# Performance work log

Hardware: AMD Instinct MI355X
Metric: run time of the kernel (lower is better)

Reference implementation:

```python
import jax, jax.numpy as jnp
import numpy as np


def reference(x, phi, sigma, M_phi_plus, M_phi_minus, M_u, padded_sl):
    """STU forward: spectral FFT convolution + autoregressive input term.

    x:   (B, L, D) input sequence
    phi: (L, K) time-domain spectral filters (top-K Hankel eigenvectors);
         V = rfft(phi, n=padded_sl) matches the module's precomputed V.
    sigma: (K,) Hankel eigenvalues
    M_phi_plus/minus: (K, D, D) per-filter projections
    M_u: (k_u, D, D) AR-on-input matrices
    """
    B, L, D = x.shape
    K = sigma.shape[0]
    n = padded_sl  # FFT length for causal linear convolution

    # Alternating-sign trick for the 'minus' featurization:
    # sum_j (-1)^j phi_j u_{t-j} = (-1)^t * conv(phi, sgn*u)_t
    sgn = jnp.where(jnp.arange(L) % 2 == 0, 1.0, -1.0).astype(x.dtype)[None, :, None]  # (1,L,1)

    V = jnp.fft.rfft(phi, n=n, axis=0)                       # (n//2+1, K) complex
    U = jnp.fft.rfft(jnp.stack([x, x * sgn], axis=-1), n=n, axis=1)  # (B, n//2+1, D, 2)
    prod = V[None, :, :, None, None] * U[:, :, None, :, :]    # (B, n//2+1, K, D, 2)
    conv = jnp.fft.irfft(prod, n=n, axis=1)[:, :L]            # (B, L, K, D, 2) causal conv
    U_plus = conv[..., 0]
    U_minus = conv[..., 1] * sgn[..., None]                   # undo sign on output side

    # Fold sigma^{1/4} scaling into the projection matrices.
    sig4 = (sigma ** 0.25).astype(x.dtype)[:, None, None]     # (K,1,1)
    spectral = (
        jnp.einsum('blkd,kdo->blo', U_plus, M_phi_plus * sig4)
        + jnp.einsum('blkd,kdo->blo', U_minus, M_phi_minus * sig4)
    )

    # compute_ar_u: y_t += sum_{i=0}^{k_u-1} x_{t-i} @ M_u[i]  (use_ar_u=True)
    ar_u = jnp.einsum('bld,do->blo', x, M_u[0])
    for i in range(1, M_u.shape[0]):  # small fixed depth k_u=3
        x_shift = jnp.pad(x, ((0, 0), (i, 0), (0, 0)))[:, :L]
        ar_u = ar_u + jnp.einsum('bld,do->blo', x_shift, M_u[i])

    # use_ar_y=False branch; dropout=0 (identity)
    return spectral + ar_u


def setup_inputs() -> dict:
    key = jax.random.key(0)
    ks = jax.random.split(key, 6)
    B, L, D, K, KU, N = 1, 2048, 768, 16, 3, 4096
    x = jax.random.normal(ks[0], (B, L, D), jnp.float32)
    phi = jax.random.normal(ks[1], (L, K), jnp.float32) / np.sqrt(L).astype(np.float32)
    sigma = jax.random.uniform(ks[2], (K,), jnp.float32, 0.1, 1.0)
    M_phi_plus = jax.random.normal(ks[3], (K, D, D), jnp.float32) * 0.02
    M_phi_minus = jax.random.normal(ks[4], (K, D, D), jnp.float32) * 0.02
    M_u = jax.random.normal(ks[5], (KU, D, D), jnp.float32) * 0.02
    return {"x": x, "phi": phi, "sigma": sigma, "M_phi_plus": M_phi_plus,
            "M_phi_minus": M_phi_minus, "M_u": M_u, "padded_sl": N}
```

## Files before the change

kernel.cpp:

```cpp
#include <hip/hip_runtime.h>

typedef __attribute__((ext_vector_type(8))) short bf16x8;
typedef __attribute__((ext_vector_type(4))) float f32x4;

#define SL 2048
#define DM 768
#define MSPEC 24576
#define MTOT  26880

__device__ __forceinline__ short f2bf(float f) {
  unsigned u = __builtin_bit_cast(unsigned, f);
  u = (u + 0x7FFFu + ((u >> 16) & 1u)) >> 16;
  return (short)u;
}

__device__ __forceinline__ void gload16(const short* g, short* l) {
  __builtin_amdgcn_global_load_lds(
      (const __attribute__((address_space(1))) void*)g,
      (__attribute__((address_space(3))) void*)l, 16, 0, 0);
}

__global__ __launch_bounds__(256) void k_front(const float* __restrict__ x,
                                               const float* __restrict__ phi,
                                               float* __restrict__ out,
                                               short* __restrict__ xT,
                                               short* __restrict__ Tmat,
                                               short* __restrict__ U) {
  __shared__ short tile[64 * 65];
  const int wid = blockIdx.x;
  const int t = threadIdx.x;

  if (wid < 1536) {
    reinterpret_cast<float4*>(out)[(size_t)wid * 256 + t] = float4{0.f, 0.f, 0.f, 0.f};

  } else if (wid < 1920) {
    const int b = wid - 1536;
    const int d0 = (b % 12) * 64, l0 = (b / 12) * 64;
#pragma unroll
    for (int rr = 0; rr < 16; ++rr) {
      int ll = rr * 4 + (t >> 6), dl = t & 63;
      tile[ll * 65 + dl] = f2bf(x[(size_t)(l0 + ll) * DM + d0 + dl]);
    }
    __syncthreads();
#pragma unroll
    for (int rr = 0; rr < 16; ++rr) {
      int dl = rr * 4 + (t >> 6), ll = t & 63;
      xT[(size_t)(d0 + dl) * SL + l0 + ll] = tile[ll * 65 + dl];
    }

  } else if (wid < 6016) {
    int g = (wid - 1920) * 256 + t;
    int b8 = g & 15, a = (g >> 4) & 127, dlag = (g >> 11) & 15, c = g >> 15;
    int k = c & 15;
    int jb = dlag * 128 + a - b8 * 8;
    short v[8];
#pragma unroll
    for (int i2 = 0; i2 < 8; ++i2) {
      int j = jb - i2;
      float p = 0.f;
      if (j >= 0) {
        p = phi[j * 16 + k];
        if (c >= 16 && (j & 1)) p = -p;
      }
      v[i2] = f2bf(p);
    }
    *reinterpret_cast<int4*>(Tmat + (size_t)g * 8) = *reinterpret_cast<const int4*>(v);

  } else {
    int g = (wid - 6016) * 256 + t;
    int d8 = g % 96;
    int rest = g / 96;
    int l = rest & 2047, i = rest >> 11;
    int d = d8 * 8;
    short v[8] = {0, 0, 0, 0, 0, 0, 0, 0};
    if (l >= i) {
      const float4* src = reinterpret_cast<const float4*>(x + (size_t)(l - i) * DM + d);
      float4 f0 = src[0], f1 = src[1];
      v[0] = f2bf(f0.x); v[1] = f2bf(f0.y); v[2] = f2bf(f0.z); v[3] = f2bf(f0.w);
      v[4] = f2bf(f1.x); v[5] = f2bf(f1.y); v[6] = f2bf(f1.z); v[7] = f2bf(f1.w);
    }
    *reinterpret_cast<int4*>(U + (size_t)l * MTOT + MSPEC + i * DM + d) =
        *reinterpret_cast<const int4*>(v);
  }
}

__global__ __launch_bounds__(256) void k_mid(const short* __restrict__ Tmat,
                                             const short* __restrict__ xT,
                                             short* __restrict__ U,
                                             const float* __restrict__ Mp,
                                             const float* __restrict__ Mm,
                                             const float* __restrict__ Mu,
                                             const float* __restrict__ sigma,
                                             short* __restrict__ McatT) {
  __shared__ __align__(16) short As[2][128 * 32];
  __shared__ __align__(16) short Bs[2][128 * 32];
  const int wid = blockIdx.x;
  const int t = threadIdx.x;

  if (wid < 3072) {
    const int slot = wid >> 3;
    const int c = (wid & 7) * 4 + (slot & 3);
    const int dtile = (slot >> 2) % 6;
    const int ib = 15 - (slot >> 2) / 6;
    const int lane = t & 63, wave = t >> 6;
    const int wm = (wave >> 1) * 64, wn = (wave & 1) * 64;
    const int lrow = lane & 15, quad = lane >> 4;
    const int l4 = lane >> 2, lq = lane & 3;
    const int r0 = wave * 32 + l4;
    const int swz = (lq ^ ((l4 >> 1) & 3)) * 8;
    const int foff = ((quad ^ ((lrow >> 1) & 3)) << 3);

    f32x4 acc[4][4] = {};
    const short* Abase = Tmat + (((size_t)c * 16) << 14) + r0 * 128 + swz;
    const short* Bbase = xT + (size_t)dtile * 128 * SL + (size_t)r0 * SL + swz;
    const int nit = 4 * (ib + 1);

    auto stage = [&](int it, int buf) {
      int dlag = it >> 2, kk = it & 3;
      const short* Ad = Abase + ((size_t)dlag << 14) + kk * 32;
      const short* Bd = Bbase + (ib - dlag) * 128 + kk * 32;
      short* lA = &As[buf][wave * 1024 + lane * 8];
      short* lB = &Bs[buf][wave * 1024 + lane * 8];
      gload16(Ad, lA);
      gload16(Ad + 16 * 128, lA + 512);
      gload16(Bd, lB);
      gload16(Bd + 16 * SL, lB + 512);
    };

    stage(0, 0);
    int cur = 0;
    for (int it = 0; it < nit; ++it) {
      __syncthreads();
      if (it + 1 < nit) stage(it + 1, cur ^ 1);
      bf16x8 af[4], bfr[4];
#pragma unroll
      for (int im = 0; im < 4; ++im)
        af[im] = *reinterpret_cast<const bf16x8*>(&As[cur][(wm + im * 16 + lrow) * 32 + foff]);
#pragma unroll
      for (int in = 0; in < 4; ++in)
        bfr[in] = *reinterpret_cast<const bf16x8*>(&Bs[cur][(wn + in * 16 + lrow) * 32 + foff]);
#pragma unroll
      for (int im = 0; im < 4; ++im)
#pragma unroll
        for (int in = 0; in < 4; ++in)
          acc[im][in] = __builtin_amdgcn_mfma_f32_16x16x32_bf16(af[im], bfr[in], acc[im][in], 0, 0, 0);
      cur ^= 1;
    }
    const int l0 = ib * 128, colbase = c * DM + dtile * 128;
#pragma unroll
    for (int im = 0; im < 4; ++im)
#pragma unroll
      for (int in = 0; in < 4; ++in)
#pragma unroll
        for (int r4 = 0; r4 < 4; ++r4) {
          int row = wm + im * 16 + quad * 4 + r4;
          int col = wn + in * 16 + lrow;
          U[(size_t)(l0 + row) * MTOT + colbase + col] = f2bf(acc[im][in][r4]);
        }

  } else {
    short* tile = &As[0][0];
    const int idx = wid - 3072;
    const int m0 = (idx % 420) * 64, o0 = (idx / 420) * 64;
#pragma unroll
    for (int rr = 0; rr < 16; ++rr) {
      int ml = rr * 4 + (t >> 6), ol = t & 63;
      int m = m0 + ml, o = o0 + ol;
      float v;
      if (m < MSPEC) {
        int c = m / DM, d = m - c * DM;
        int k = c & 15;
        float s4 = sqrtf(sqrtf(sigma[k]));
        if (c < 16) v = Mp[((size_t)c * DM + d) * DM + o] * s4;
        else        v = Mm[((size_t)(c - 16) * DM + d) * DM + o] * s4;
      } else {
        int mm = m - MSPEC;
        int i = mm / DM, d = mm - i * DM;
        v = Mu[((size_t)i * DM + d) * DM + o];
      }
      tile[ml * 65 + ol] = f2bf(v);
    }
    __syncthreads();
#pragma unroll
    for (int rr = 0; rr < 16; ++rr) {
      int ol = rr * 4 + (t >> 6), ml = t & 63;
      McatT[(size_t)(o0 + ol) * MTOT + m0 + ml] = tile[ml * 65 + ol];
    }
  }
}

__global__ __launch_bounds__(256) void k_gemm2(const short* __restrict__ U,
                                               const short* __restrict__ McatT,
                                               float* __restrict__ out) {
  __shared__ __align__(16) short As[2][128 * 32];
  __shared__ __align__(16) short Bs[2][128 * 32];
  const int wid = blockIdx.x;
  const int kc = wid & 7;
  const int slot = wid >> 3;
  const int otile = slot % 6;
  const int lb = slot / 6;
  const int t = threadIdx.x;
  const int lane = t & 63, wave = t >> 6;
  const int wm = (wave >> 1) * 64, wn = (wave & 1) * 64;
  const int lrow = lane & 15, quad = lane >> 4;
  const int l4 = lane >> 2, lq = lane & 3;
  const int r0 = wave * 32 + l4;
  const int swz = (lq ^ ((l4 >> 1) & 3)) * 8;
  const int foff = ((quad ^ ((lrow >> 1) & 3)) << 3);

  f32x4 acc[4][4] = {};
  const short* Ab = U + (size_t)lb * 128 * MTOT + kc * 3360 + (size_t)r0 * MTOT + swz;
  const short* Bb = McatT + (size_t)otile * 128 * MTOT + kc * 3360 + (size_t)r0 * MTOT + swz;

  auto stage = [&](int s, int buf) {
    short* lA = &As[buf][wave * 1024 + lane * 8];
    short* lB = &Bs[buf][wave * 1024 + lane * 8];
    gload16(Ab + s * 32, lA);
    gload16(Ab + s * 32 + (size_t)16 * MTOT, lA + 512);
    gload16(Bb + s * 32, lB);
    gload16(Bb + s * 32 + (size_t)16 * MTOT, lB + 512);
  };

  stage(0, 0);
  int cur = 0;
  for (int s = 0; s < 105; ++s) {
    __syncthreads();
    if (s + 1 < 105) stage(s + 1, cur ^ 1);
    bf16x8 af[4], bfr[4];
#pragma unroll
    for (int im = 0; im < 4; ++im)
      af[im] = *reinterpret_cast<const bf16x8*>(&As[cur][(wm + im * 16 + lrow) * 32 + foff]);
#pragma unroll
    for (int in = 0; in < 4; ++in)
      bfr[in] = *reinterpret_cast<const bf16x8*>(&Bs[cur][(wn + in * 16 + lrow) * 32 + foff]);
#pragma unroll
    for (int im = 0; im < 4; ++im)
#pragma unroll
      for (int in = 0; in < 4; ++in)
        acc[im][in] = __builtin_amdgcn_mfma_f32_16x16x32_bf16(af[im], bfr[in], acc[im][in], 0, 0, 0);
    cur ^= 1;
  }
  const int l0 = lb * 128, o0 = otile * 128;
#pragma unroll
  for (int im = 0; im < 4; ++im)
#pragma unroll
    for (int in = 0; in < 4; ++in)
#pragma unroll
      for (int r4 = 0; r4 < 4; ++r4) {
        int row = wm + im * 16 + quad * 4 + r4;
        int col = wn + in * 16 + lrow;
        atomicAdd(&out[(size_t)(l0 + row) * DM + o0 + col], acc[im][in][r4]);
      }
}

extern "C" void kernel_launch(void* const* d_in, const int* in_sizes, int n_in,
                              void* d_out, int out_size, void* d_ws, size_t ws_size,
                              hipStream_t stream) {
  (void)in_sizes; (void)n_in; (void)out_size; (void)ws_size;
  const float* x     = (const float*)d_in[0];
  const float* phi   = (const float*)d_in[1];
  const float* sigma = (const float*)d_in[2];
  const float* Mp    = (const float*)d_in[3];
  const float* Mm    = (const float*)d_in[4];
  const float* Mu    = (const float*)d_in[5];
  float* out = (float*)d_out;
  char* ws = (char*)d_ws;

  short* U     = (short*)(ws);
  short* Tmat  = (short*)(ws + 110100480);
  short* xT    = (short*)(ws + 126877696);
  short* McatT = (short*)(ws + 130023424);

  k_front<<<dim3(8320), dim3(256), 0, stream>>>(x, phi, out, xT, Tmat, U);
  k_mid<<<dim3(8112), dim3(256), 0, stream>>>(Tmat, xT, U, Mp, Mm, Mu, sigma, McatT);
  k_gemm2<<<dim3(768), dim3(256), 0, stream>>>(U, McatT, out);
}
```

Before: 444.2 us.

## Fuse spectral GEMM and output GEMM with per-row-block counters for overlap

The McatT transpose/scale work moves into the front kernel, and the Toeplitz GEMM and the projection GEMM are merged into one launch. Output GEMM blocks spin on a per-L-block completion counter that the first-stage blocks increment, so output GEMM work for finished row blocks can overlap the remaining first-stage work. This removes one launch and the tail bubble between the stages. It relies on forward-progress assumptions about block scheduling, since the higher-index waiting blocks must not starve the producers, and it adds spin-wait overhead.

```diff
diff --git a/kernel.cpp b/kernel.cpp
--- a/kernel.cpp
+++ b/kernel.cpp
@@ -7,6 +7,7 @@
 #define DM 768
 #define MSPEC 24576
 #define MTOT  26880
+#define CNT_OFF 171311104
 
 __device__ __forceinline__ short f2bf(float f) {
   unsigned u = __builtin_bit_cast(unsigned, f);
@@ -22,146 +23,22 @@
 
 __global__ __launch_bounds__(256) void k_front(const float* __restrict__ x,
                                                const float* __restrict__ phi,
+                                               const float* __restrict__ Mp,
+                                               const float* __restrict__ Mm,
+                                               const float* __restrict__ Mu,
+                                               const float* __restrict__ sigma,
                                                float* __restrict__ out,
                                                short* __restrict__ xT,
                                                short* __restrict__ Tmat,
-                                               short* __restrict__ U) {
+                                               short* __restrict__ U,
+                                               short* __restrict__ McatT,
+                                               unsigned* __restrict__ cnt) {
   __shared__ short tile[64 * 65];
   const int wid = blockIdx.x;
   const int t = threadIdx.x;
 
-  if (wid < 1536) {
-    reinterpret_cast<float4*>(out)[(size_t)wid * 256 + t] = float4{0.f, 0.f, 0.f, 0.f};
-
-  } else if (wid < 1920) {
-    const int b = wid - 1536;
-    const int d0 = (b % 12) * 64, l0 = (b / 12) * 64;
-#pragma unroll
-    for (int rr = 0; rr < 16; ++rr) {
-      int ll = rr * 4 + (t >> 6), dl = t & 63;
-      tile[ll * 65 + dl] = f2bf(x[(size_t)(l0 + ll) * DM + d0 + dl]);
-    }
-    __syncthreads();
-#pragma unroll
-    for (int rr = 0; rr < 16; ++rr) {
-      int dl = rr * 4 + (t >> 6), ll = t & 63;
-      xT[(size_t)(d0 + dl) * SL + l0 + ll] = tile[ll * 65 + dl];
-    }
-
-  } else if (wid < 6016) {
-    int g = (wid - 1920) * 256 + t;
-    int b8 = g & 15, a = (g >> 4) & 127, dlag = (g >> 11) & 15, c = g >> 15;
-    int k = c & 15;
-    int jb = dlag * 128 + a - b8 * 8;
-    short v[8];
-#pragma unroll
-    for (int i2 = 0; i2 < 8; ++i2) {
-      int j = jb - i2;
-      float p = 0.f;
-      if (j >= 0) {
-        p = phi[j * 16 + k];
-        if (c >= 16 && (j & 1)) p = -p;
-      }
-      v[i2] = f2bf(p);
-    }
-    *reinterpret_cast<int4*>(Tmat + (size_t)g * 8) = *reinterpret_cast<const int4*>(v);
-
-  } else {
-    int g = (wid - 6016) * 256 + t;
-    int d8 = g % 96;
-    int rest = g / 96;
-    int l = rest & 2047, i = rest >> 11;
-    int d = d8 * 8;
-    short v[8] = {0, 0, 0, 0, 0, 0, 0, 0};
-    if (l >= i) {
-      const float4* src = reinterpret_cast<const float4*>(x + (size_t)(l - i) * DM + d);
-      float4 f0 = src[0], f1 = src[1];
-      v[0] = f2bf(f0.x); v[1] = f2bf(f0.y); v[2] = f2bf(f0.z); v[3] = f2bf(f0.w);
-      v[4] = f2bf(f1.x); v[5] = f2bf(f1.y); v[6] = f2bf(f1.z); v[7] = f2bf(f1.w);
-    }
-    *reinterpret_cast<int4*>(U + (size_t)l * MTOT + MSPEC + i * DM + d) =
-        *reinterpret_cast<const int4*>(v);
-  }
-}
-
-__global__ __launch_bounds__(256) void k_mid(const short* __restrict__ Tmat,
-                                             const short* __restrict__ xT,
-                                             short* __restrict__ U,
-                                             const float* __restrict__ Mp,
-                                             const float* __restrict__ Mm,
-                                             const float* __restrict__ Mu,
-                                             const float* __restrict__ sigma,
-                                             short* __restrict__ McatT) {
-  __shared__ __align__(16) short As[2][128 * 32];
-  __shared__ __align__(16) short Bs[2][128 * 32];
-  const int wid = blockIdx.x;
-  const int t = threadIdx.x;
-
-  if (wid < 3072) {
-    const int slot = wid >> 3;
-    const int c = (wid & 7) * 4 + (slot & 3);
-    const int dtile = (slot >> 2) % 6;
-    const int ib = 15 - (slot >> 2) / 6;
-    const int lane = t & 63, wave = t >> 6;
-    const int wm = (wave >> 1) * 64, wn = (wave & 1) * 64;
-    const int lrow = lane & 15, quad = lane >> 4;
-    const int l4 = lane >> 2, lq = lane & 3;
-    const int r0 = wave * 32 + l4;
-    const int swz = (lq ^ ((l4 >> 1) & 3)) * 8;
-    const int foff = ((quad ^ ((lrow >> 1) & 3)) << 3);
-
-    f32x4 acc[4][4] = {};
-    const short* Abase = Tmat + (((size_t)c * 16) << 14) + r0 * 128 + swz;
-    const short* Bbase = xT + (size_t)dtile * 128 * SL + (size_t)r0 * SL + swz;
-    const int nit = 4 * (ib + 1);
-
-    auto stage = [&](int it, int buf) {
-      int dlag = it >> 2, kk = it & 3;
-      const short* Ad = Abase + ((size_t)dlag << 14) + kk * 32;
-      const short* Bd = Bbase + (ib - dlag) * 128 + kk * 32;
-      short* lA = &As[buf][wave * 1024 + lane * 8];
-      short* lB = &Bs[buf][wave * 1024 + lane * 8];
-      gload16(Ad, lA);
-      gload16(Ad + 16 * 128, lA + 512);
-      gload16(Bd, lB);
-      gload16(Bd + 16 * SL, lB + 512);
-    };
-
-    stage(0, 0);
-    int cur = 0;
-    for (int it = 0; it < nit; ++it) {
-      __syncthreads();
-      if (it + 1 < nit) stage(it + 1, cur ^ 1);
-      bf16x8 af[4], bfr[4];
-#pragma unroll
-      for (int im = 0; im < 4; ++im)
-        af[im] = *reinterpret_cast<const bf16x8*>(&As[cur][(wm + im * 16 + lrow) * 32 + foff]);
-#pragma unroll
-      for (int in = 0; in < 4; ++in)
-        bfr[in] = *reinterpret_cast<const bf16x8*>(&Bs[cur][(wn + in * 16 + lrow) * 32 + foff]);
-#pragma unroll
-      for (int im = 0; im < 4; ++im)
-#pragma unroll
-        for (int in = 0; in < 4; ++in)
-          acc[im][in] = __builtin_amdgcn_mfma_f32_16x16x32_bf16(af[im], bfr[in], acc[im][in], 0, 0, 0);
-      cur ^= 1;
-    }
-    const int l0 = ib * 128, colbase = c * DM + dtile * 128;
-#pragma unroll
-    for (int im = 0; im < 4; ++im)
-#pragma unroll
-      for (int in = 0; in < 4; ++in)
-#pragma unroll
-        for (int r4 = 0; r4 < 4; ++r4) {
-          int row = wm + im * 16 + quad * 4 + r4;
-          int col = wn + in * 16 + lrow;
-          U[(size_t)(l0 + row) * MTOT + colbase + col] = f2bf(acc[im][in][r4]);
-        }
-
-  } else {
-    short* tile = &As[0][0];
-    const int idx = wid - 3072;
-    const int m0 = (idx % 420) * 64, o0 = (idx / 420) * 64;
+  if (wid < 5040) {
+    const int m0 = (wid % 420) * 64, o0 = (wid / 420) * 64;
 #pragma unroll
     for (int rr = 0; rr < 16; ++rr) {
       int ml = rr * 4 + (t >> 6), ol = t & 63;
@@ -186,19 +63,72 @@
       int ol = rr * 4 + (t >> 6), ml = t & 63;
       McatT[(size_t)(o0 + ol) * MTOT + m0 + ml] = tile[ml * 65 + ol];
     }
+
+  } else if (wid < 6576) {
+    const int w2 = wid - 5040;
+    if (w2 == 0 && t < 16) cnt[t] = 0u;
+    reinterpret_cast<float4*>(out)[(size_t)w2 * 256 + t] = float4{0.f, 0.f, 0.f, 0.f};
+
+  } else if (wid < 6960) {
+    const int b = wid - 6576;
+    const int d0 = (b % 12) * 64, l0 = (b / 12) * 64;
+#pragma unroll
+    for (int rr = 0; rr < 16; ++rr) {
+      int ll = rr * 4 + (t >> 6), dl = t & 63;
+      tile[ll * 65 + dl] = f2bf(x[(size_t)(l0 + ll) * DM + d0 + dl]);
+    }
+    __syncthreads();
+#pragma unroll
+    for (int rr = 0; rr < 16; ++rr) {
+      int dl = rr * 4 + (t >> 6), ll = t & 63;
+      xT[(size_t)(d0 + dl) * SL + l0 + ll] = tile[ll * 65 + dl];
+    }
+
+  } else if (wid < 11056) {
+    int g = (wid - 6960) * 256 + t;
+    int b8 = g & 15, a = (g >> 4) & 127, dlag = (g >> 11) & 15, c = g >> 15;
+    int k = c & 15;
+    int jb = dlag * 128 + a - b8 * 8;
+    short v[8];
+#pragma unroll
+    for (int i2 = 0; i2 < 8; ++i2) {
+      int j = jb - i2;
+      float p = 0.f;
+      if (j >= 0) {
+        p = phi[j * 16 + k];
+        if (c >= 16 && (j & 1)) p = -p;
+      }
+      v[i2] = f2bf(p);
+    }
+    *reinterpret_cast<int4*>(Tmat + (size_t)g * 8) = *reinterpret_cast<const int4*>(v);
+
+  } else {
+    int g = (wid - 11056) * 256 + t;
+    int d8 = g % 96;
+    int rest = g / 96;
+    int l = rest & 2047, i = rest >> 11;
+    int d = d8 * 8;
+    short v[8] = {0, 0, 0, 0, 0, 0, 0, 0};
+    if (l >= i) {
+      const float4* src = reinterpret_cast<const float4*>(x + (size_t)(l - i) * DM + d);
+      float4 f0 = src[0], f1 = src[1];
+      v[0] = f2bf(f0.x); v[1] = f2bf(f0.y); v[2] = f2bf(f0.z); v[3] = f2bf(f0.w);
+      v[4] = f2bf(f1.x); v[5] = f2bf(f1.y); v[6] = f2bf(f1.z); v[7] = f2bf(f1.w);
+    }
+    *reinterpret_cast<int4*>(U + (size_t)l * MTOT + MSPEC + i * DM + d) =
+        *reinterpret_cast<const int4*>(v);
   }
 }
 
-__global__ __launch_bounds__(256) void k_gemm2(const short* __restrict__ U,
-                                               const short* __restrict__ McatT,
-                                               float* __restrict__ out) {
+__global__ __launch_bounds__(256) void k_gemm12(const short* __restrict__ Tmat,
+                                                const short* __restrict__ xT,
+                                                short* __restrict__ U,
+                                                const short* __restrict__ McatT,
+                                                float* __restrict__ out,
+                                                unsigned* __restrict__ cnt) {
   __shared__ __align__(16) short As[2][128 * 32];
   __shared__ __align__(16) short Bs[2][128 * 32];
   const int wid = blockIdx.x;
-  const int kc = wid & 7;
-  const int slot = wid >> 3;
-  const int otile = slot % 6;
-  const int lb = slot / 6;
   const int t = threadIdx.x;
   const int lane = t & 63, wave = t >> 6;
   const int wm = (wave >> 1) * 64, wn = (wave & 1) * 64;
@@ -207,50 +137,125 @@
   const int r0 = wave * 32 + l4;
   const int swz = (lq ^ ((l4 >> 1) & 3)) * 8;
   const int foff = ((quad ^ ((lrow >> 1) & 3)) << 3);
-
   f32x4 acc[4][4] = {};
-  const short* Ab = U + (size_t)lb * 128 * MTOT + kc * 3360 + (size_t)r0 * MTOT + swz;
-  const short* Bb = McatT + (size_t)otile * 128 * MTOT + kc * 3360 + (size_t)r0 * MTOT + swz;
-
-  auto stage = [&](int s, int buf) {
-    short* lA = &As[buf][wave * 1024 + lane * 8];
-    short* lB = &Bs[buf][wave * 1024 + lane * 8];
-    gload16(Ab + s * 32, lA);
-    gload16(Ab + s * 32 + (size_t)16 * MTOT, lA + 512);
-    gload16(Bb + s * 32, lB);
-    gload16(Bb + s * 32 + (size_t)16 * MTOT, lB + 512);
-  };
-
-  stage(0, 0);
-  int cur = 0;
-  for (int s = 0; s < 105; ++s) {
-    __syncthreads();
-    if (s + 1 < 105) stage(s + 1, cur ^ 1);
-    bf16x8 af[4], bfr[4];
+
+  if (wid < 3072) {
+    const int slot = wid >> 3;
+    const int c = (wid & 7) * 4 + (slot & 3);
+    const int dtile = (slot >> 2) % 6;
+    const int ib = 15 - (slot >> 2) / 6;
+
+    const short* Abase = Tmat + (((size_t)c * 16) << 14) + r0 * 128 + swz;
+    const short* Bbase = xT + (size_t)dtile * 128 * SL + (size_t)r0 * SL + swz;
+    const int nit = 4 * (ib + 1);
+
+    auto stage = [&](int it, int buf) {
+      int dlag = it >> 2, kk = it & 3;
+      const short* Ad = Abase + ((size_t)dlag << 14) + kk * 32;
+      const short* Bd = Bbase + (ib - dlag) * 128 + kk * 32;
+      short* lA = &As[buf][wave * 1024 + lane * 8];
+      short* lB = &Bs[buf][wave * 1024 + lane * 8];
+      gload16(Ad, lA);
+      gload16(Ad + 16 * 128, lA + 512);
+      gload16(Bd, lB);
+      gload16(Bd + 16 * SL, lB + 512);
+    };
+
+    stage(0, 0);
+    int cur = 0;
+    for (int it = 0; it < nit; ++it) {
+      __syncthreads();
+      if (it + 1 < nit) stage(it + 1, cur ^ 1);
+      bf16x8 af[4], bfr[4];
+#pragma unroll
+      for (int im = 0; im < 4; ++im)
+        af[im] = *reinterpret_cast<const bf16x8*>(&As[cur][(wm + im * 16 + lrow) * 32 + foff]);
+#pragma unroll
+      for (int in = 0; in < 4; ++in)
+        bfr[in] = *reinterpret_cast<const bf16x8*>(&Bs[cur][(wn + in * 16 + lrow) * 32 + foff]);
+#pragma unroll
+      for (int im = 0; im < 4; ++im)
+#pragma unroll
+        for (int in = 0; in < 4; ++in)
+          acc[im][in] = __builtin_amdgcn_mfma_f32_16x16x32_bf16(af[im], bfr[in], acc[im][in], 0, 0, 0);
+      cur ^= 1;
+    }
+    const int l0 = ib * 128, colbase = c * DM + dtile * 128;
 #pragma unroll
     for (int im = 0; im < 4; ++im)
-      af[im] = *reinterpret_cast<const bf16x8*>(&As[cur][(wm + im * 16 + lrow) * 32 + foff]);
-#pragma unroll
-    for (int in = 0; in < 4; ++in)
-      bfr[in] = *reinterpret_cast<const bf16x8*>(&Bs[cur][(wn + in * 16 + lrow) * 32 + foff]);
+#pragma unroll
+      for (int in = 0; in < 4; ++in)
+#pragma unroll
+        for (int r4 = 0; r4 < 4; ++r4) {
+          int row = wm + im * 16 + quad * 4 + r4;
+          int col = wn + in * 16 + lrow;
+          U[(size_t)(l0 + row) * MTOT + colbase + col] = f2bf(acc[im][in][r4]);
+        }
+    __syncthreads();
+    if (t == 0) {
+      __threadfence();
+      __hip_atomic_fetch_add(&cnt[ib], 1u, __ATOMIC_RELEASE, __HIP_MEMORY_SCOPE_AGENT);
+    }
+
+  } else {
+    const int bid = wid - 3072;
+    const int kc = bid & 7;
+    const int slot = bid >> 3;
+    const int otile = slot % 6;
+    const int lb = 15 - slot / 6;
+
+    if (t == 0) {
+      long spins = 0;
+      while (__hip_atomic_load(&cnt[lb], __ATOMIC_ACQUIRE, __HIP_MEMORY_SCOPE_AGENT) < 192u) {
+        __builtin_amdgcn_s_sleep(32);
+        if (++spins > 100000000L) break;
+      }
+    }
+    __syncthreads();
+
+    const short* Ab = U + (size_t)lb * 128 * MTOT + kc * 3360 + (size_t)r0 * MTOT + swz;
+    const short* Bb = McatT + (size_t)otile * 128 * MTOT + kc * 3360 + (size_t)r0 * MTOT + swz;
+
+    auto stage = [&](int s, int buf) {
+      short* lA = &As[buf][wave * 1024 + lane * 8];
+      short* lB = &Bs[buf][wave * 1024 + lane * 8];
+      gload16(Ab + s * 32, lA);
+      gload16(Ab + s * 32 + (size_t)16 * MTOT, lA + 512);
+      gload16(Bb + s * 32, lB);
+      gload16(Bb + s * 32 + (size_t)16 * MTOT, lB + 512);
+    };
+
+    stage(0, 0);
+    int cur = 0;
+    for (int s = 0; s < 105; ++s) {
+      __syncthreads();
+      if (s + 1 < 105) stage(s + 1, cur ^ 1);
+      bf16x8 af[4], bfr[4];
+#pragma unroll
+      for (int im = 0; im < 4; ++im)
+        af[im] = *reinterpret_cast<const bf16x8*>(&As[cur][(wm + im * 16 + lrow) * 32 + foff]);
+#pragma unroll
+      for (int in = 0; in < 4; ++in)
+        bfr[in] = *reinterpret_cast<const bf16x8*>(&Bs[cur][(wn + in * 16 + lrow) * 32 + foff]);
+#pragma unroll
+      for (int im = 0; im < 4; ++im)
+#pragma unroll
+        for (int in = 0; in < 4; ++in)
+          acc[im][in] = __builtin_amdgcn_mfma_f32_16x16x32_bf16(af[im], bfr[in], acc[im][in], 0, 0, 0);
+      cur ^= 1;
+    }
+    const int l0 = lb * 128, o0 = otile * 128;
 #pragma unroll
     for (int im = 0; im < 4; ++im)
 #pragma unroll
       for (int in = 0; in < 4; ++in)
-        acc[im][in] = __builtin_amdgcn_mfma_f32_16x16x32_bf16(af[im], bfr[in], acc[im][in], 0, 0, 0);
-    cur ^= 1;
+#pragma unroll
+        for (int r4 = 0; r4 < 4; ++r4) {
+          int row = wm + im * 16 + quad * 4 + r4;
+          int col = wn + in * 16 + lrow;
+          atomicAdd(&out[(size_t)(l0 + row) * DM + o0 + col], acc[im][in][r4]);
+        }
   }
-  const int l0 = lb * 128, o0 = otile * 128;
-#pragma unroll
-  for (int im = 0; im < 4; ++im)
-#pragma unroll
-    for (int in = 0; in < 4; ++in)
-#pragma unroll
-      for (int r4 = 0; r4 < 4; ++r4) {
-        int row = wm + im * 16 + quad * 4 + r4;
-        int col = wn + in * 16 + lrow;
-        atomicAdd(&out[(size_t)(l0 + row) * DM + o0 + col], acc[im][in][r4]);
-      }
 }
 
 extern "C" void kernel_launch(void* const* d_in, const int* in_sizes, int n_in,
@@ -266,12 +271,13 @@
   float* out = (float*)d_out;
   char* ws = (char*)d_ws;
 
-  short* U     = (short*)(ws);
-  short* Tmat  = (short*)(ws + 110100480);
-  short* xT    = (short*)(ws + 126877696);
-  short* McatT = (short*)(ws + 130023424);
-
-  k_front<<<dim3(8320), dim3(256), 0, stream>>>(x, phi, out, xT, Tmat, U);
-  k_mid<<<dim3(8112), dim3(256), 0, stream>>>(Tmat, xT, U, Mp, Mm, Mu, sigma, McatT);
-  k_gemm2<<<dim3(768), dim3(256), 0, stream>>>(U, McatT, out);
-}
+  short* U        = (short*)(ws);
+  short* Tmat     = (short*)(ws + 110100480);
+  short* xT       = (short*)(ws + 126877696);
+  short* McatT    = (short*)(ws + 130023424);
+  unsigned* cnt   = (unsigned*)(ws + CNT_OFF);
+
+  k_front<<<dim3(13360), dim3(256), 0, stream>>>(x, phi, Mp, Mm, Mu, sigma,
+                                                 out, xT, Tmat, U, McatT, cnt);
+  k_gemm12<<<dim3(3840), dim3(256), 0, stream>>>(Tmat, xT, U, McatT, out, cnt);
+}
```

After: 738.4 us. 1.66x slower.
